# Kernel optimization log

Hardware: AMD Instinct MI355X
Metric: run time of the kernel (lower is better)

The kernel has to match this reference:

```python
import jax, jax.numpy as jnp
import numpy as np

LAMBDA_SOFTMAX = 20.0  # opt.lambda_softmax
EPS = 1e-8
NEG = -1e30


def l2norm(x, axis):
    # torch l2norm: x / (sqrt(sum x^2) + eps)
    n = jnp.sqrt(jnp.sum(x * x, axis=axis, keepdims=True)) + EPS
    return x / n


def cosine(x1, x2, axis):
    # torch compute_similarity: sum(x1*x2)/clamp(|x1||x2|, min=eps)
    w12 = jnp.sum(x1 * x2, axis=axis)
    w1 = jnp.sqrt(jnp.sum(x1 * x1, axis=axis))
    w2 = jnp.sqrt(jnp.sum(x2 * x2, axis=axis))
    return w12 / jnp.maximum(w1 * w2, EPS)


def _focal_renorm(a, sourceL):
    # focal_equal: fattn = 1[a*S - sum(a) > 0], then renormalize fattn*a
    funcF = a * sourceL - jnp.sum(a, axis=-1, keepdims=True)
    fattn = jnp.where(funcF > 0, 1.0, 0.0)
    ta = fattn * a
    s = jnp.sum(ta, axis=-1, keepdims=True)
    return ta / jnp.where(s > 0, s, 1.0)


def compute_weiTexts(img_q, img_v, txt_k_all, txt_v_all, text_length):
    N, R, d = img_q.shape          # n_img, n_region, d
    Lw = txt_k_all.shape[1]        # max words
    qn_img = l2norm(img_q, -1)     # [N,R,d]
    mask_all = (jnp.arange(Lw)[None, :] < text_length[:, None])  # [T,Lw] bool

    def per_text(txt_k, txt_v, mask, n_word):
        # mask out padded words (torch slices [:n_word])
        m = mask.astype(txt_k.dtype)[:, None]        # [Lw,1]
        tk = l2norm(txt_k * m, -1)                   # [Lw,d], padded rows -> 0
        tv = txt_v * m                                # [Lw,d]

        # ---- i2t: query=img, context=text (sourceL = n_word) ----
        attn = jnp.einsum('ld,nrd->nlr', tk, qn_img)  # bmm(key_norm, queryT) [N,Lw,R]
        attn = jax.nn.leaky_relu(attn, 0.1)
        attn = l2norm(attn, 2)                        # over R
        attn = jnp.transpose(attn, (0, 2, 1))         # [N,R,Lw]
        logits = jnp.where(mask[None, None, :], attn * LAMBDA_SOFTMAX, NEG)
        a = jax.nn.softmax(logits, axis=-1)           # [N,R,Lw]
        a = _focal_renorm(a, n_word)
        wei_text = jnp.einsum('nrl,ld->nrd', a, tv)   # [N,R,d]
        wei_text = l2norm(wei_text, 2)
        i2t = jnp.mean(cosine(img_v, wei_text, 2), axis=1)  # [N]

        # ---- t2i: query=text, context=img (sourceL = R) ----
        attn2 = jnp.einsum('nrd,ld->nrl', qn_img, tk)  # bmm(key_norm, queryT) [N,R,Lw]
        attn2 = jax.nn.leaky_relu(attn2, 0.1)
        attn2 = l2norm(attn2, 2)                       # over Lw (padded cols are 0)
        attn2 = jnp.transpose(attn2, (0, 2, 1))        # [N,Lw,R]
        a2 = jax.nn.softmax(attn2 * LAMBDA_SOFTMAX, axis=-1)
        a2 = _focal_renorm(a2, float(R))
        wei_img = jnp.einsum('nlr,nrd->nld', a2, img_v)  # [N,Lw,d]
        wei_img = l2norm(wei_img, 2)
        cos2 = cosine(tv[None, :, :], wei_img, 2)        # [N,Lw]; padded rows -> 0
        t2i = jnp.sum(cos2 * mask.astype(cos2.dtype)[None, :], axis=1) / n_word
        return i2t, t2i

    n_word_f = text_length.astype(img_q.dtype)
    i2t_T, t2i_T = jax.vmap(per_text)(txt_k_all, txt_v_all, mask_all, n_word_f)
    # loop concatenated along dim 1 -> [n_img, n_txt]
    return i2t_T.T, t2i_T.T


def setup_inputs() -> dict:
    key = jax.random.key(0)
    k1, k2, k3, k4, k5 = jax.random.split(key, 5)
    N, T, R, Lw, d = 128, 128, 48, 64, 1024
    return {
        'local_img_query': jax.random.normal(k1, (N, R, d), dtype=jnp.float32),
        'local_img_value': jax.random.normal(k2, (N, R, d), dtype=jnp.float32),
        'local_text_key': jax.random.normal(k3, (T, Lw, d), dtype=jnp.float32),
        'local_text_value': jax.random.normal(k4, (T, Lw, d), dtype=jnp.float32),
        'text_length': jax.random.randint(k5, (T,), 16, Lw + 1, dtype=jnp.int32),
    }


def reference(local_img_query, local_img_value, local_text_key, local_text_value, text_length):
    return compute_weiTexts(local_img_query, local_img_value,
                            local_text_key, local_text_value, text_length)
```

## Files before the change

kernel.cpp:

```cpp
#include <hip/hip_runtime.h>

#define NIMG 128
#define NTXT 128
#define RDIM 48
#define LWRD 64
#define DDIM 1024
#define LAMB 20.0f
#define FEPS 1e-8f

#define WS_INVQ 0
#define WS_VN   6144
#define WS_INVK 12288
#define WS_TVN  20480
#define WS_H    28672
#define WS_VG   552960
#define WS_MID_BYTES 3391488ull
#define WS_HU   847872
#define WS_VGU  1372160
#define SP_TK   3334144
#define SP_TV   20111360
#define SP_Q    36888576
#define SP_V    49471488
#define WS_BIG_BYTES 124108800ull

typedef unsigned int u32;
typedef __attribute__((ext_vector_type(8))) short short8;
typedef __attribute__((ext_vector_type(4))) float f32x4;
typedef __attribute__((ext_vector_type(4))) u32 uintx4;
typedef __attribute__((ext_vector_type(2))) u32 uintx2;

#define MFMA(a,b,c) __builtin_amdgcn_mfma_f32_16x16x32_bf16(a,b,c,0,0,0)

__device__ __forceinline__ u32 f2bf(float x){
    u32 u = __float_as_uint(x);
    return (u + 0x7fffu + ((u >> 16) & 1u)) >> 16;
}
__device__ __forceinline__ float bf2f(u32 h){ return __uint_as_float(h << 16); }
__device__ __forceinline__ u32 packsplit(float x){
    u32 h = f2bf(x);
    u32 l = f2bf(x - bf2f(h));
    return h | (l << 16);
}
__device__ __forceinline__ void unpk(uintx4 a, uintx4 b, short8& hi, short8& lo){
    uintx4 h, l;
    h.x = (a.x & 0xffffu) | (a.y << 16);
    h.y = (a.z & 0xffffu) | (a.w << 16);
    h.z = (b.x & 0xffffu) | (b.y << 16);
    h.w = (b.z & 0xffffu) | (b.w << 16);
    l.x = (a.x >> 16) | (a.y & 0xffff0000u);
    l.y = (a.z >> 16) | (a.w & 0xffff0000u);
    l.z = (b.x >> 16) | (b.y & 0xffff0000u);
    l.w = (b.z >> 16) | (b.w & 0xffff0000u);
    hi = __builtin_bit_cast(short8, h);
    lo = __builtin_bit_cast(short8, l);
}

#define PSTR  40
#define PTKH  0
#define PTVH  2560
#define PQH   5120
#define PVH   8960
#define LOGAP 12800
__device__ __forceinline__ void split_store(short* stg, int idx, float4 x, float sc){
    float a0 = x.x*sc, a1 = x.y*sc, a2 = x.z*sc, a3 = x.w*sc;
    u32 h0=f2bf(a0), h1=f2bf(a1), h2=f2bf(a2), h3=f2bf(a3);
    u32 l0=f2bf(a0-bf2f(h0)), l1=f2bf(a1-bf2f(h1)), l2=f2bf(a2-bf2f(h2)), l3=f2bf(a3-bf2f(h3));
    uintx2 hv; hv.x = h0 | (h1<<16); hv.y = h2 | (h3<<16);
    uintx2 lv; lv.x = l0 | (l1<<16); lv.y = l2 | (l3<<16);
    *(uintx2*)(stg + idx)         = hv;
    *(uintx2*)(stg + idx + LOGAP) = lv;
}
__device__ __forceinline__ short8 frag_ld(const short* stg, int plane, int rb, int m16, int quad){
    return *(const short8*)(stg + plane + (rb + m16) * PSTR + quad * 8);
}

__global__ __launch_bounds__(256, 2)
void prep_norms(const float* __restrict__ imq, const float* __restrict__ imv,
                const float* __restrict__ txk, const float* __restrict__ txv,
                float* __restrict__ ws) {
    int vid = blockIdx.x * 4 + (threadIdx.x >> 6);
    int lane = threadIdx.x & 63;
    const float* src;
    if (vid < 6144)       src = imq + (size_t)vid * 1024;
    else if (vid < 12288) src = imv + (size_t)(vid - 6144) * 1024;
    else if (vid < 20480) src = txk + (size_t)(vid - 12288) * 1024;
    else                  src = txv + (size_t)(vid - 20480) * 1024;
    const float4* s4 = (const float4*)src;
    float acc = 0.f;
#pragma unroll
    for (int j = 0; j < 4; ++j) {
        float4 v = s4[lane + 64 * j];
        acc += v.x * v.x + v.y * v.y + v.z * v.z + v.w * v.w;
    }
#pragma unroll
    for (int off = 32; off; off >>= 1) acc += __shfl_down(acc, off, 64);
    if (lane == 0) {
        float nrm = sqrtf(acc);
        if (vid < 6144)       ws[vid] = 1.f / (nrm + FEPS);
        else if (vid < 12288) ws[vid] = nrm;
        else if (vid < 20480) ws[vid] = 1.f / (nrm + FEPS);
        else                  ws[vid] = nrm;
    }
}

__global__ __launch_bounds__(256, 2)
void split_kernel(const float* __restrict__ imq, const float* __restrict__ imv,
                  const float* __restrict__ txk, const float* __restrict__ txv,
                  const int* __restrict__ tlen, const float* __restrict__ wsf,
                  short* __restrict__ wss) {
    const int ten = blockIdx.y;
    const int jid = blockIdx.x * 256 + threadIdx.x;
    const float* src; float sc; size_t dst; int psz;
    if (ten < 2) {
        int slab = jid >> 13, r = jid & 8191;
        int kc = r >> 8, row = (r >> 2) & 63, ks = r & 3;
        const float* base = (ten == 0) ? txk : txv;
        src = base + (size_t)slab * 65536 + row * 1024 + kc * 32 + ks * 8;
        int nw = tlen[slab];
        if (ten == 0) sc = (row < nw) ? wsf[WS_INVK + slab * 64 + row] : 0.f;
        else          sc = (row < nw) ? 1.f : 0.f;
        dst = (size_t)(ten == 0 ? SP_TK : SP_TV) + (size_t)slab * 131072
            + kc * 2048 + row * 32 + ks * 8;
        psz = 65536;
    } else {
        if (jid >= 786432) return;
        int slab = jid / 6144, r = jid - slab * 6144;
        int kc = r / 192; int rr = r - kc * 192;
        int row = rr >> 2, ks = rr & 3;
        const float* base = (ten == 2) ? imq : imv;
        src = base + (size_t)slab * 49152 + row * 1024 + kc * 32 + ks * 8;
        sc = (ten == 2) ? wsf[WS_INVQ + slab * 48 + row] : 1.f;
        dst = (size_t)(ten == 2 ? SP_Q : SP_V) + (size_t)slab * 98304
            + kc * 1536 + row * 32 + ks * 8;
        psz = 49152;
    }
    float4 x0 = *(const float4*)src;
    float4 x1 = *(const float4*)(src + 4);
    float v[8] = {x0.x, x0.y, x0.z, x0.w, x1.x, x1.y, x1.z, x1.w};
    short8 hv, lv;
#pragma unroll
    for (int i = 0; i < 8; ++i) {
        float a = v[i] * sc;
        u32 h = f2bf(a);
        hv[i] = (short)h;
        lv[i] = (short)f2bf(a - bf2f(h));
    }
    *(short8*)(wss + dst) = hv;
    *(short8*)(wss + dst + psz) = lv;
}

template <int TS>
__device__ __forceinline__ void gram_body(const float* __restrict__ src,
                                          float* __restrict__ dstf,
                                          u32* __restrict__ dstu,
                                          int mode, int nw, float* sT){
    const int NR = TS * 16;
    int ar = threadIdx.x >> 4, ac = threadIdx.x & 15;
    float acc[TS][TS];
#pragma unroll
    for (int i = 0; i < TS; ++i)
#pragma unroll
        for (int j = 0; j < TS; ++j) acc[i][j] = 0.f;
    for (int kc = 0; kc < 8; ++kc) {
        int k0 = kc * 128;
        for (int jid = threadIdx.x; jid < NR * 32; jid += 256) {
            int row = jid >> 5, c4 = jid & 31;
            float4 x = *(const float4*)(src + row * 1024 + k0 + c4 * 4);
            float sc = (row < nw) ? 1.f : 0.f;
            x.x *= sc; x.y *= sc; x.z *= sc; x.w *= sc;
            *(float4*)&sT[row * 132 + c4 * 4] = x;
        }
        __syncthreads();
#pragma unroll 4
        for (int k4 = 0; k4 < 32; ++k4) {
            float4 av[TS], bv[TS];
#pragma unroll
            for (int i = 0; i < TS; ++i) av[i] = *(const float4*)&sT[(TS*ar + i) * 132 + k4 * 4];
#pragma unroll
            for (int j = 0; j < TS; ++j) bv[j] = *(const float4*)&sT[(TS*ac + j) * 132 + k4 * 4];
#pragma unroll
            for (int i = 0; i < TS; ++i)
#pragma unroll
                for (int j = 0; j < TS; ++j)
                    acc[i][j] += av[i].x*bv[j].x + av[i].y*bv[j].y + av[i].z*bv[j].z + av[i].w*bv[j].w;
        }
        __syncthreads();
    }
#pragma unroll
    for (int i = 0; i < TS; ++i)
#pragma unroll
        for (int j = 0; j < TS; ++j) {
            int idx = (TS*ar + i) * NR + TS*ac + j;
            if (mode) dstu[idx] = packsplit(acc[i][j]);
            else      dstf[idx] = acc[i][j];
        }
}

__global__ __launch_bounds__(256, 2)
void gram_kernel(const float* __restrict__ txv, const float* __restrict__ imv,
                 const int* __restrict__ tlen, float* __restrict__ ws, int mode){
    __shared__ __align__(16) float sT[64 * 132];
    int b = blockIdx.x;
    u32* wsu = (u32*)ws;
    if (b < 128) {
        gram_body<4>(txv + (size_t)b * 65536, ws + WS_H + (size_t)b * 4096,
                     wsu + WS_HU + (size_t)b * 4096, mode, tlen[b], sT);
    } else {
        int n = b - 128;
        gram_body<3>(imv + (size_t)n * 49152, ws + WS_VG + (size_t)n * 2304,
                     wsu + WS_VGU + (size_t)n * 2304, mode, 48, sT);
    }
}

__global__ __launch_bounds__(256, 4)
void loss_mfma3(const int* __restrict__ tlen, const float* __restrict__ ws,
                float* __restrict__ out) {
    const int n    = blockIdx.x;
    const int t    = blockIdx.y;
    const int tid  = threadIdx.x;
    const int lane = tid & 63;
    const int w    = tid >> 6;
    const int quad = lane >> 4;
    const int m16  = lane & 15;

    __shared__ __align__(16) float Sm[10064];
    u32*   A1w = (u32*)Sm;
    u32*   A2w = ((u32*)Sm) + 3264;
    short* stg = (short*)Sm;
    float* P   = Sm + 6592;
    float* sNl = Sm + 9728;
    float* sNr = Sm + 9792;
    float* sD1 = Sm + 9840;
    float* sS1 = Sm + 9888;
    float* sD2 = Sm + 9936;
    float* sS2 = Sm + 10000;

    const int nw = tlen[t];
    const float nwf = (float)nw;
    const short* wss = (const short*)ws;
    const u32*   wsu = (const u32*)ws;

    const short* bsrc[3]; int bdst[3];
#pragma unroll
    for (int it = 0; it < 3; ++it) {
        int jid = tid + 256 * it;
        int p = jid / 192; int rr = jid - p * 192;
        int row = rr >> 2, ks = rr & 3;
        bsrc[it] = wss + (p < 2 ? SP_Q : SP_V) + (size_t)n * 98304
                 + (size_t)(p & 1) * 49152 + row * 32 + ks * 8;
        bdst[it] = p * 1920 + row * 40 + ks * 8;
    }

    const short* tkh = wss + SP_TK + (size_t)t * 131072;
    const short* tkl = tkh + 65536;
    const short* tvh = wss + SP_TV + (size_t)t * 131072;
    const short* tvl = tvh + 65536;
    const int ar = (16 * w + m16) * 32 + quad * 8;

    f32x4 accS[3], accG[3];
    f32x4 zf = {0.f, 0.f, 0.f, 0.f};
#pragma unroll
    for (int j = 0; j < 3; ++j) { accS[j] = zf; accG[j] = zf; }

    short8 bj[3];
#pragma unroll
    for (int it = 0; it < 3; ++it) bj[it] = *(const short8*)(bsrc[it]);
    short8 kh0, kl0, th0, tl0, kh1, kl1, th1, tl1;
    kh0 = *(const short8*)(tkh + ar); kl0 = *(const short8*)(tkl + ar);
    th0 = *(const short8*)(tvh + ar); tl0 = *(const short8*)(tvl + ar);

    for (int kc2 = 0; kc2 < 16; ++kc2) {
        const int kc = kc2 * 2;
        {
#pragma unroll
            for (int it = 0; it < 3; ++it) *(short8*)(stg + bdst[it]) = bj[it];
            __syncthreads();
            int bo = (kc + 1) * 1536, ao = (kc + 1) * 2048 + ar;
#pragma unroll
            for (int it = 0; it < 3; ++it) bj[it] = *(const short8*)(bsrc[it] + bo);
            kh1 = *(const short8*)(tkh + ao); kl1 = *(const short8*)(tkl + ao);
            th1 = *(const short8*)(tvh + ao); tl1 = *(const short8*)(tvl + ao);
#pragma unroll
            for (int j = 0; j < 3; ++j) {
                int o = (16 * j + m16) * 40 + quad * 8;
                short8 bqh = *(const short8*)(stg + o);
                short8 bql = *(const short8*)(stg + 1920 + o);
                short8 bvh = *(const short8*)(stg + 3840 + o);
                short8 bvl = *(const short8*)(stg + 5760 + o);
                accS[j] = MFMA(kh0, bqh, accS[j]);
                accS[j] = MFMA(kh0, bql, accS[j]);
                accS[j] = MFMA(kl0, bqh, accS[j]);
                accG[j] = MFMA(th0, bvh, accG[j]);
                accG[j] = MFMA(th0, bvl, accG[j]);
                accG[j] = MFMA(tl0, bvh, accG[j]);
            }
            __syncthreads();
        }
        {
#pragma unroll
            for (int it = 0; it < 3; ++it) *(short8*)(stg + bdst[it]) = bj[it];
            __syncthreads();
            if (kc2 < 15) {
                int bo = (kc + 2) * 1536, ao = (kc + 2) * 2048 + ar;
#pragma unroll
                for (int it = 0; it < 3; ++it) bj[it] = *(const short8*)(bsrc[it] + bo);
                kh0 = *(const short8*)(tkh + ao); kl0 = *(const short8*)(tkl + ao);
                th0 = *(const short8*)(tvh + ao); tl0 = *(const short8*)(tvl + ao);
            }
#pragma unroll
            for (int j = 0; j < 3; ++j) {
                int o = (16 * j + m16) * 40 + quad * 8;
                short8 bqh = *(const short8*)(stg + o);
                short8 bql = *(const short8*)(stg + 1920 + o);
                short8 bvh = *(const short8*)(stg + 3840 + o);
                short8 bvl = *(const short8*)(stg + 5760 + o);
                accS[j] = MFMA(kh1, bqh, accS[j]);
                accS[j] = MFMA(kh1, bql, accS[j]);
                accS[j] = MFMA(kl1, bqh, accS[j]);
                accG[j] = MFMA(th1, bvh, accG[j]);
                accG[j] = MFMA(th1, bvl, accG[j]);
                accG[j] = MFMA(tl1, bvh, accG[j]);
            }
            __syncthreads();
        }
    }

#pragma unroll
    for (int j = 0; j < 3; ++j)
#pragma unroll
        for (int v = 0; v < 4; ++v) {
            int l = 16 * w + quad * 4 + v;
            float x = accS[j][v];
            P[l * 49 + 16 * j + m16] = (x > 0.f) ? x : 0.1f * x;
        }
    __syncthreads();

    if (tid < 64) {
        float s = 0.f;
#pragma unroll 4
        for (int r = 0; r < 48; ++r) { float x = P[tid * 49 + r]; s += x * x; }
        sNl[tid] = sqrtf(s) + FEPS;
    } else if (tid < 112) {
        int r = tid - 64;
        float s = 0.f;
#pragma unroll 4
        for (int l = 0; l < 64; ++l) { float x = P[l * 49 + r]; s += x * x; }
        sNr[r] = sqrtf(s) + FEPS;
    } else if (tid < 208) {
        int k = tid - 112;
        if (k < 48) sD1[k] = 0.f; else sS1[k - 48] = 0.f;
    }
    __syncthreads();

    if (tid < 64) {
        int l = tid;
        u32* row = A2w + l * 52;
        if (l < nw) {
            float a[48]; float mx = -1e30f;
            const float* Pr = P + l * 49;
#pragma unroll
            for (int r = 0; r < 48; ++r) {
                float x = LAMB * Pr[r] / sNr[r];
                a[r] = x; mx = fmaxf(mx, x);
            }
            float se = 0.f;
#pragma unroll
            for (int r = 0; r < 48; ++r) { float e = __expf(a[r] - mx); a[r] = e; se += e; }
            float suma = 0.f;
#pragma unroll
            for (int r = 0; r < 48; ++r) { float x = a[r] / se; a[r] = x; suma += x; }
            float s2 = 0.f;
#pragma unroll
            for (int r = 0; r < 48; ++r) if (a[r] * 48.f - suma > 0.f) s2 += a[r];
            float ri = (s2 > 0.f) ? 1.f / s2 : 1.f;
#pragma unroll
            for (int r = 0; r < 48; ++r) {
                float x = (a[r] * 48.f - suma > 0.f) ? a[r] * ri : 0.f;
                row[r] = packsplit(x);
            }
        } else {
#pragma unroll
            for (int r = 0; r < 48; ++r) row[r] = 0u;
        }
    } else if (tid < 112) {
        int r = tid - 64;
        float a[64]; float mx = -1e30f;
#pragma unroll
        for (int l = 0; l < 64; ++l) {
            float x = (l < nw) ? (LAMB * P[l * 49 + r] / sNl[l]) : -1e30f;
            a[l] = x; mx = fmaxf(mx, x);
        }
        float se = 0.f;
#pragma unroll
        for (int l = 0; l < 64; ++l) { float e = __expf(a[l] - mx); a[l] = e; se += e; }
        float suma = 0.f;
#pragma unroll
        for (int l = 0; l < 64; ++l) { float x = a[l] / se; a[l] = x; suma += x; }
        float s2 = 0.f;
#pragma unroll
        for (int l = 0; l < 64; ++l) if (a[l] * nwf - suma > 0.f) s2 += a[l];
        float ri = (s2 > 0.f) ? 1.f / s2 : 1.f;
        u32* row = A1w + r * 68;
#pragma unroll
        for (int l = 0; l < 64; ++l) {
            float x = (a[l] * nwf - suma > 0.f) ? a[l] * ri : 0.f;
            row[l] = packsplit(x);
        }
    }
    __syncthreads();

    f32x4 accY[3];
#pragma unroll
    for (int j = 0; j < 3; ++j) accY[j] = zf;
    const u32* Hg = wsu + WS_HU + (size_t)t * 4096 + (16 * w + m16) * 64;
#pragma unroll
    for (int ks = 0; ks < 2; ++ks) {
        int kb = ks * 32 + quad * 8;
        short8 Ah, Al;
        {
            uintx4 wa = *(const uintx4*)&Hg[kb];
            uintx4 wb = *(const uintx4*)&Hg[kb + 4];
            unpk(wa, wb, Ah, Al);
        }
#pragma unroll
        for (int j = 0; j < 3; ++j) {
            int base = (16 * j + m16) * 68 + kb;
            uintx4 wa = *(const uintx4*)&A1w[base];
            uintx4 wb = *(const uintx4*)&A1w[base + 4];
            short8 Bh, Bl;
            unpk(wa, wb, Bh, Bl);
            accY[j] = MFMA(Ah, Bh, accY[j]);
            accY[j] = MFMA(Ah, Bl, accY[j]);
            accY[j] = MFMA(Al, Bh, accY[j]);
        }
    }
    {
        float td[3] = {0.f, 0.f, 0.f}, ts[3] = {0.f, 0.f, 0.f};
#pragma unroll
        for (int v = 0; v < 4; ++v) {
            int l = 16 * w + quad * 4 + v;
#pragma unroll
            for (int j = 0; j < 3; ++j) {
                u32 wv = A1w[(16 * j + m16) * 68 + l];
                float av = bf2f(wv & 0xffffu) + bf2f(wv >> 16);
                td[j] += av * accG[j][v];
                ts[j] += av * accY[j][v];
            }
        }
#pragma unroll
        for (int j = 0; j < 3; ++j) {
            float d = td[j]; d += __shfl_xor(d, 16, 64); d += __shfl_xor(d, 32, 64);
            float s = ts[j]; s += __shfl_xor(s, 16, 64); s += __shfl_xor(s, 32, 64);
            if (quad == 0) {
                atomicAdd(&sD1[16 * j + m16], d);
                atomicAdd(&sS1[16 * j + m16], s);
            }
        }
    }

    f32x4 accY2[3];
#pragma unroll
    for (int i = 0; i < 3; ++i) accY2[i] = zf;
    const u32* Vgg = wsu + WS_VGU + (size_t)n * 2304;
#pragma unroll
    for (int ks = 0; ks < 2; ++ks) {
        const bool dead = (ks == 1) && (quad >= 2);
        const int kb = (ks == 0) ? quad * 8 : 32 + (quad & 1) * 8;
        short8 Bh2, Bl2;
        {
            uintx4 wa = {0,0,0,0}, wb = {0,0,0,0};
            if (!dead) {
                int base = (16 * w + m16) * 52 + kb;
                wa = *(const uintx4*)&A2w[base];
                wb = *(const uintx4*)&A2w[base + 4];
            }
            unpk(wa, wb, Bh2, Bl2);
        }
#pragma unroll
        for (int i = 0; i < 3; ++i) {
            uintx4 wa = {0,0,0,0}, wb = {0,0,0,0};
            if (!dead) {
                wa = *(const uintx4*)&Vgg[(16 * i + m16) * 48 + kb];
                wb = *(const uintx4*)&Vgg[(16 * i + m16) * 48 + kb + 4];
            }
            short8 Ah2, Al2;
            unpk(wa, wb, Ah2, Al2);
            accY2[i] = MFMA(Ah2, Bh2, accY2[i]);
            accY2[i] = MFMA(Ah2, Bl2, accY2[i]);
            accY2[i] = MFMA(Al2, Bh2, accY2[i]);
        }
    }
    {
        float u = 0.f;
#pragma unroll
        for (int i = 0; i < 3; ++i)
#pragma unroll
            for (int v = 0; v < 4; ++v) {
                int r = 16 * i + quad * 4 + v;
                u32 wv = A2w[(16 * w + m16) * 52 + r];
                float av = bf2f(wv & 0xffffu) + bf2f(wv >> 16);
                u += av * accY2[i][v];
            }
        u += __shfl_xor(u, 16, 64); u += __shfl_xor(u, 32, 64);
        if (quad == 0) sS2[16 * w + m16] = u;
        float ud[4] = {0.f, 0.f, 0.f, 0.f};
#pragma unroll
        for (int v = 0; v < 4; ++v) {
            int l = 16 * w + quad * 4 + v;
#pragma unroll
            for (int j = 0; j < 3; ++j) {
                u32 wv = A2w[l * 52 + 16 * j + m16];
                float av = bf2f(wv & 0xffffu) + bf2f(wv >> 16);
                ud[v] += av * accG[j][v];
            }
        }
#pragma unroll
        for (int v = 0; v < 4; ++v) {
            float d = ud[v];
            d += __shfl_xor(d, 1, 64); d += __shfl_xor(d, 2, 64);
            d += __shfl_xor(d, 4, 64); d += __shfl_xor(d, 8, 64);
            if (m16 == 0) sD2[16 * w + quad * 4 + v] = d;
        }
    }
    __syncthreads();

    if (tid < 48) {
        int r = tid;
        float wn = sqrtf(sS1[r]);
        float dh = sD1[r] / (wn + FEPS);
        float nh = wn / (wn + FEPS);
        float vn = ws[WS_VN + n * 48 + r];
        sD1[r] = dh / fmaxf(vn * nh, FEPS);
    } else if (tid >= 64 && tid < 128) {
        int l = tid - 64;
        if (l < nw) {
            float wn = sqrtf(sS2[l]);
            float dh = sD2[l] / (wn + FEPS);
            float nh = wn / (wn + FEPS);
            float tn = ws[WS_TVN + t * 64 + l];
            sD2[l] = dh / fmaxf(tn * nh, FEPS);
        }
    }
    __syncthreads();
    if (tid == 0) {
        float s = 0.f;
        for (int r = 0; r < 48; ++r) s += sD1[r];
        out[(size_t)n * NTXT + t] = s / 48.f;
    } else if (tid == 64) {
        float s = 0.f;
        for (int l = 0; l < nw; ++l) s += sD2[l];
        out[(size_t)(NIMG * NTXT) + (size_t)n * NTXT + t] = s / nwf;
    }
}

__global__ __launch_bounds__(256, 2)
void loss_mfma(const float* __restrict__ imq, const float* __restrict__ imv,
               const float* __restrict__ txk, const float* __restrict__ txv,
               const int* __restrict__ tlen, const float* __restrict__ ws,
               float* __restrict__ out) {
    const int npair = blockIdx.x;
    const int t     = blockIdx.y;
    const int n0    = npair * 2;
    const int tid   = threadIdx.x;
    const int lane  = tid & 63;
    const int w     = tid >> 6;
    const int nl    = w >> 1;
    const int hh    = w & 1;
    const int quad  = lane >> 4;
    const int m16   = lane & 15;

    __shared__ __align__(16) float Sm[19904];
    short* stage = (short*)Sm;
    u32*   A1w   = (u32*)Sm;
    u32*   A2w   = ((u32*)Sm) + 6528;
    float* P     = Sm + 12800;
    u32*   HVw   = (u32*)(Sm + 12800);
    float* sInvK = Sm + 19072;
    float* sInvQ = sInvK + 64;
    float* sNl   = sInvQ + 96;
    float* sNr   = sNl + 128;
    float* sD1   = sNr + 96;
    float* sS1   = sD1 + 96;
    float* sD2   = sS1 + 96;
    float* sS2   = sD2 + 128;

    const int nw = tlen[t];
    const float nwf = (float)nw;
    if (tid < 64) sInvK[tid] = ws[WS_INVK + t * 64 + tid];
    else if (tid < 160) {
        int i = tid - 64; int nn = i >= 48; int r = i - 48 * nn;
        sInvQ[i] = ws[WS_INVQ + (n0 + nn) * 48 + r];
    }
    __syncthreads();

    const float* tkb = txk + (size_t)t * 65536;
    const float* tvb = txv + (size_t)t * 65536;
    const float* qb0 = imq + (size_t)n0 * 49152;
    const float* vb0 = imv + (size_t)n0 * 49152;

    const float* sp[10]; int di[10]; float scl[10];
#pragma unroll
    for (int it = 0; it < 10; ++it) {
        int jid = tid + 256 * it;
        const float* s; int plane; int row, c4; float sc;
        if (it < 2) {
            row = jid >> 3; c4 = jid & 7;
            s = tkb + row * 1024 + c4 * 4;
            sc = (row < nw) ? sInvK[row] : 0.f;
            plane = PTKH;
        } else if (it < 4) {
            int j2 = jid - 512; row = j2 >> 3; c4 = j2 & 7;
            s = tvb + row * 1024 + c4 * 4;
            sc = (row < nw) ? 1.f : 0.f;
            plane = PTVH;
        } else if (it < 7) {
            int j2 = jid - 1024; row = j2 >> 3; c4 = j2 & 7;
            s = qb0 + row * 1024 + c4 * 4;
            sc = sInvQ[row];
            plane = PQH;
        } else {
            int j2 = jid - 1792; row = j2 >> 3; c4 = j2 & 7;
            s = vb0 + row * 1024 + c4 * 4;
            sc = 1.f;
            plane = PVH;
        }
        sp[it] = s; di[it] = plane + row * PSTR + c4 * 4; scl[it] = sc;
    }

    f32x4 accS[2][3], accG[2][3];
    f32x4 zf = {0.f, 0.f, 0.f, 0.f};
#pragma unroll
    for (int i = 0; i < 2; ++i)
#pragma unroll
        for (int j = 0; j < 3; ++j) { accS[i][j] = zf; accG[i][j] = zf; }

    float4 pf[10];
#pragma unroll
    for (int it = 0; it < 10; ++it) pf[it] = *(const float4*)(sp[it]);

    for (int kc = 0; kc < 32; ++kc) {
#pragma unroll
        for (int it = 0; it < 10; ++it) split_store(stage, di[it], pf[it], scl[it]);
        __syncthreads();
        if (kc < 31) {
            const int ko = (kc + 1) * 32;
#pragma unroll
            for (int it = 0; it < 10; ++it) pf[it] = *(const float4*)(sp[it] + ko);
        }
        short8 akh[2], akl[2], ath[2], atl[2];
#pragma unroll
        for (int i = 0; i < 2; ++i) {
            int rb = 32 * hh + 16 * i;
            akh[i] = frag_ld(stage, PTKH,         rb, m16, quad);
            akl[i] = frag_ld(stage, PTKH + LOGAP, rb, m16, quad);
            ath[i] = frag_ld(stage, PTVH,         rb, m16, quad);
            atl[i] = frag_ld(stage, PTVH + LOGAP, rb, m16, quad);
        }
        short8 bqh[3], bql[3], bvh[3], bvl[3];
#pragma unroll
        for (int j = 0; j < 3; ++j) {
            int rb = nl * 48 + 16 * j;
            bqh[j] = frag_ld(stage, PQH,         rb, m16, quad);
            bql[j] = frag_ld(stage, PQH + LOGAP, rb, m16, quad);
            bvh[j] = frag_ld(stage, PVH,         rb, m16, quad);
            bvl[j] = frag_ld(stage, PVH + LOGAP, rb, m16, quad);
        }
#pragma unroll
        for (int i = 0; i < 2; ++i)
#pragma unroll
            for (int j = 0; j < 3; ++j) {
                accS[i][j] = MFMA(akh[i], bqh[j], accS[i][j]);
                accS[i][j] = MFMA(akh[i], bql[j], accS[i][j]);
                accS[i][j] = MFMA(akl[i], bqh[j], accS[i][j]);
                accG[i][j] = MFMA(ath[i], bvh[j], accG[i][j]);
                accG[i][j] = MFMA(ath[i], bvl[j], accG[i][j]);
                accG[i][j] = MFMA(atl[i], bvh[j], accG[i][j]);
            }
        __syncthreads();
    }

#pragma unroll
    for (int i = 0; i < 2; ++i)
#pragma unroll
        for (int j = 0; j < 3; ++j)
#pragma unroll
            for (int v = 0; v < 4; ++v) {
                int l = 32 * hh + 16 * i + quad * 4 + v;
                int r = 16 * j + m16;
                float x = accS[i][j][v];
                P[nl * 3136 + l * 49 + r] = (x > 0.f) ? x : 0.1f * x;
            }
    __syncthreads();

    if (tid < 128) {
        int n = tid >> 6, l = tid & 63;
        float s = 0.f;
#pragma unroll 4
        for (int r = 0; r < 48; ++r) { float x = P[n*3136 + l*49 + r]; s += x * x; }
        sNl[n * 64 + l] = sqrtf(s) + FEPS;
    } else if (tid < 224) {
        int i = tid - 128; int n = i >= 48; int r = i - 48 * n;
        float s = 0.f;
#pragma unroll 4
        for (int l = 0; l < 64; ++l) { float x = P[n*3136 + l*49 + r]; s += x * x; }
        sNr[n * 48 + r] = sqrtf(s) + FEPS;
    } else {
        for (int k = tid - 224; k < 448; k += 32) sD1[k] = 0.f;
    }
    __syncthreads();

    if (tid < 128) {
        int n = tid >> 6, l = tid & 63;
        u32* row = A2w + n * 3072 + l * 48;
        if (l < nw) {
            float a[48]; float mx = -1e30f;
            const float* Pr = P + n * 3136 + l * 49;
#pragma unroll
            for (int r = 0; r < 48; ++r) {
                float x = LAMB * Pr[r] / sNr[n * 48 + r];
                a[r] = x; mx = fmaxf(mx, x);
            }
            float se = 0.f;
#pragma unroll
            for (int r = 0; r < 48; ++r) { float e = __expf(a[r] - mx); a[r] = e; se += e; }
            float suma = 0.f;
#pragma unroll
            for (int r = 0; r < 48; ++r) { float x = a[r] / se; a[r] = x; suma += x; }
            float s2 = 0.f;
#pragma unroll
            for (int r = 0; r < 48; ++r) if (a[r] * 48.f - suma > 0.f) s2 += a[r];
            float ri = (s2 > 0.f) ? 1.f / s2 : 1.f;
#pragma unroll
            for (int r = 0; r < 48; ++r) {
                float x = (a[r] * 48.f - suma > 0.f) ? a[r] * ri : 0.f;
                row[r] = packsplit(x);
            }
        } else {
#pragma unroll
            for (int r = 0; r < 48; ++r) row[r] = 0u;
        }
    } else if (tid < 224) {
        int i = tid - 128; int n = i >= 48; int r = i - 48 * n;
        float a[64]; float mx = -1e30f;
#pragma unroll
        for (int l = 0; l < 64; ++l) {
            float x = (l < nw) ? (LAMB * P[n*3136 + l*49 + r] / sNl[n * 64 + l]) : -1e30f;
            a[l] = x; mx = fmaxf(mx, x);
        }
        float se = 0.f;
#pragma unroll
        for (int l = 0; l < 64; ++l) { float e = __expf(a[l] - mx); a[l] = e; se += e; }
        float suma = 0.f;
#pragma unroll
        for (int l = 0; l < 64; ++l) { float x = a[l] / se; a[l] = x; suma += x; }
        float s2 = 0.f;
#pragma unroll
        for (int l = 0; l < 64; ++l) if (a[l] * nwf - suma > 0.f) s2 += a[l];
        float ri = (s2 > 0.f) ? 1.f / s2 : 1.f;
        u32* row = A1w + n * 3264 + r * 68;
#pragma unroll
        for (int l = 0; l < 64; ++l) {
            float x = (a[l] * nwf - suma > 0.f) ? a[l] * ri : 0.f;
            row[l] = packsplit(x);
        }
    }
    __syncthreads();

    {
        const float* Hg = ws + WS_H + (size_t)t * 4096;
        for (int jid = tid; jid < 1024; jid += 256) {
            int row = jid >> 4, c4 = jid & 15;
            float4 x = *(const float4*)(Hg + row * 64 + c4 * 4);
            uintx4 p; p.x = packsplit(x.x); p.y = packsplit(x.y);
            p.z = packsplit(x.z); p.w = packsplit(x.w);
            *(uintx4*)&HVw[row * 68 + c4 * 4] = p;
        }
    }
    __syncthreads();

    f32x4 accY[2][3];
#pragma unroll
    for (int i = 0; i < 2; ++i)
#pragma unroll
        for (int j = 0; j < 3; ++j) accY[i][j] = zf;
#pragma unroll
    for (int ks = 0; ks < 2; ++ks) {
        int kb = ks * 32 + quad * 8;
        short8 Ah[2], Al[2];
#pragma unroll
        for (int i = 0; i < 2; ++i) {
            int row = 32 * hh + 16 * i + m16;
            uintx4 wa = *(const uintx4*)&HVw[row * 68 + kb];
            uintx4 wb = *(const uintx4*)&HVw[row * 68 + kb + 4];
            unpk(wa, wb, Ah[i], Al[i]);
        }
        short8 Bh[3], Bl[3];
#pragma unroll
        for (int j = 0; j < 3; ++j) {
            int base = nl * 3264 + (16 * j + m16) * 68 + kb;
            uintx4 wa = *(const uintx4*)&A1w[base];
            uintx4 wb = *(const uintx4*)&A1w[base + 4];
            unpk(wa, wb, Bh[j], Bl[j]);
        }
#pragma unroll
        for (int i = 0; i < 2; ++i)
#pragma unroll
            for (int j = 0; j < 3; ++j) {
                accY[i][j] = MFMA(Ah[i], Bh[j], accY[i][j]);
                accY[i][j] = MFMA(Ah[i], Bl[j], accY[i][j]);
                accY[i][j] = MFMA(Al[i], Bh[j], accY[i][j]);
            }
    }
    {
        float td[3] = {0.f, 0.f, 0.f}, ts[3] = {0.f, 0.f, 0.f};
#pragma unroll
        for (int i = 0; i < 2; ++i)
#pragma unroll
            for (int v = 0; v < 4; ++v) {
                int l = 32 * hh + 16 * i + quad * 4 + v;
#pragma unroll
                for (int j = 0; j < 3; ++j) {
                    u32 wv = A1w[nl * 3264 + (16 * j + m16) * 68 + l];
                    float av = bf2f(wv & 0xffffu) + bf2f(wv >> 16);
                    td[j] += av * accG[i][j][v];
                    ts[j] += av * accY[i][j][v];
                }
            }
#pragma unroll
        for (int j = 0; j < 3; ++j) {
            float d = td[j]; d += __shfl_xor(d, 16, 64); d += __shfl_xor(d, 32, 64);
            float s = ts[j]; s += __shfl_xor(s, 16, 64); s += __shfl_xor(s, 32, 64);
            if (quad == 0) {
                atomicAdd(&sD1[nl * 48 + 16 * j + m16], d);
                atomicAdd(&sS1[nl * 48 + 16 * j + m16], s);
            }
        }
    }
    __syncthreads();

    {
        const float* Vgg = ws + WS_VG + (size_t)n0 * 2304;
        for (int jid = tid; jid < 1152; jid += 256) {
            int nn = jid >= 576; int j2 = jid - 576 * nn;
            int row = j2 / 12, c4 = j2 % 12;
            float4 x = *(const float4*)(Vgg + nn * 2304 + row * 48 + c4 * 4);
            uintx4 p; p.x = packsplit(x.x); p.y = packsplit(x.y);
            p.z = packsplit(x.z); p.w = packsplit(x.w);
            *(uintx4*)&HVw[nn * 2496 + row * 52 + c4 * 4] = p;
        }
    }
    __syncthreads();

    f32x4 accY2[3][2];
#pragma unroll
    for (int i = 0; i < 3; ++i)
#pragma unroll
        for (int j = 0; j < 2; ++j) accY2[i][j] = zf;
    const u32* VgW = HVw + nl * 2496;
#pragma unroll
    for (int ks = 0; ks < 2; ++ks) {
        const bool dead = (ks == 1) && (quad >= 2);
        const int kb = (ks == 0) ? quad * 8 : 32 + (quad & 1) * 8;
        short8 Ah2[3], Al2[3];
#pragma unroll
        for (int i = 0; i < 3; ++i) {
            uintx4 wa = {0,0,0,0}, wb = {0,0,0,0};
            if (!dead) {
                int row = 16 * i + m16;
                wa = *(const uintx4*)&VgW[row * 52 + kb];
                wb = *(const uintx4*)&VgW[row * 52 + kb + 4];
            }
            unpk(wa, wb, Ah2[i], Al2[i]);
        }
        short8 Bh2[2], Bl2[2];
#pragma unroll
        for (int j = 0; j < 2; ++j) {
            uintx4 wa = {0,0,0,0}, wb = {0,0,0,0};
            if (!dead) {
                int l = 32 * hh + 16 * j + m16;
                wa = *(const uintx4*)&A2w[nl * 3072 + l * 48 + kb];
                wb = *(const uintx4*)&A2w[nl * 3072 + l * 48 + kb + 4];
            }
            unpk(wa, wb, Bh2[j], Bl2[j]);
        }
#pragma unroll
        for (int i = 0; i < 3; ++i)
#pragma unroll
            for (int j = 0; j < 2; ++j) {
                accY2[i][j] = MFMA(Ah2[i], Bh2[j], accY2[i][j]);
                accY2[i][j] = MFMA(Ah2[i], Bl2[j], accY2[i][j]);
                accY2[i][j] = MFMA(Al2[i], Bh2[j], accY2[i][j]);
            }
    }
    {
        float u[2] = {0.f, 0.f};
#pragma unroll
        for (int i = 0; i < 3; ++i)
#pragma unroll
            for (int v = 0; v < 4; ++v) {
                int r = 16 * i + quad * 4 + v;
#pragma unroll
                for (int j = 0; j < 2; ++j) {
                    int l = 32 * hh + 16 * j + m16;
                    u32 wv = A2w[nl * 3072 + l * 48 + r];
                    float av = bf2f(wv & 0xffffu) + bf2f(wv >> 16);
                    u[j] += av * accY2[i][j][v];
                }
            }
#pragma unroll
        for (int j = 0; j < 2; ++j) {
            float s = u[j]; s += __shfl_xor(s, 16, 64); s += __shfl_xor(s, 32, 64);
            if (quad == 0) sS2[nl * 64 + 32 * hh + 16 * j + m16] = s;
        }
        float ud[2][4];
#pragma unroll
        for (int i = 0; i < 2; ++i)
#pragma unroll
            for (int v = 0; v < 4; ++v) ud[i][v] = 0.f;
#pragma unroll
        for (int i = 0; i < 2; ++i)
#pragma unroll
            for (int v = 0; v < 4; ++v) {
                int l = 32 * hh + 16 * i + quad * 4 + v;
#pragma unroll
                for (int j = 0; j < 3; ++j) {
                    u32 wv = A2w[nl * 3072 + l * 48 + (16 * j + m16)];
                    float av = bf2f(wv & 0xffffu) + bf2f(wv >> 16);
                    ud[i][v] += av * accG[i][j][v];
                }
            }
#pragma unroll
        for (int i = 0; i < 2; ++i)
#pragma unroll
            for (int v = 0; v < 4; ++v) {
                float d = ud[i][v];
                d += __shfl_xor(d, 1, 64); d += __shfl_xor(d, 2, 64);
                d += __shfl_xor(d, 4, 64); d += __shfl_xor(d, 8, 64);
                if (m16 == 0) sD2[nl * 64 + 32 * hh + 16 * i + quad * 4 + v] = d;
            }
    }
    __syncthreads();

    if (tid < 96) {
        int n = tid >= 48; int r = tid - 48 * n;
        float wn = sqrtf(sS1[n * 48 + r]);
        float dh = sD1[n * 48 + r] / (wn + FEPS);
        float nh = wn / (wn + FEPS);
        float vn = ws[WS_VN + (n0 + n) * 48 + r];
        sD1[n * 48 + r] = dh / fmaxf(vn * nh, FEPS);
    } else if (tid >= 128) {
        int i = tid - 128; int n = i >> 6, l = i & 63;
        if (l < nw) {
            float wn = sqrtf(sS2[n * 64 + l]);
            float dh = sD2[n * 64 + l] / (wn + FEPS);
            float nh = wn / (wn + FEPS);
            float tn = ws[WS_TVN + t * 64 + l];
            sD2[n * 64 + l] = dh / fmaxf(tn * nh, FEPS);
        }
    }
    __syncthreads();
    if (tid < 2) {
        float s = 0.f;
        for (int r = 0; r < 48; ++r) s += sD1[tid * 48 + r];
        out[(size_t)(n0 + tid) * NTXT + t] = s / 48.f;
    } else if (tid == 64 || tid == 65) {
        int n = tid - 64;
        float s = 0.f;
        for (int l = 0; l < nw; ++l) s += sD2[n * 64 + l];
        out[(size_t)(NIMG * NTXT) + (size_t)(n0 + n) * NTXT + t] = s / nwf;
    }
}

extern "C" void kernel_launch(void* const* d_in, const int* in_sizes, int n_in,
                              void* d_out, int out_size, void* d_ws, size_t ws_size,
                              hipStream_t stream) {
    (void)in_sizes; (void)n_in; (void)out_size;
    const float* imq = (const float*)d_in[0];
    const float* imv = (const float*)d_in[1];
    const float* txk = (const float*)d_in[2];
    const float* txv = (const float*)d_in[3];
    const int*   tln = (const int*)d_in[4];
    float* out = (float*)d_out;
    float* ws  = (float*)d_ws;

    prep_norms<<<7168, 256, 0, stream>>>(imq, imv, txk, txv, ws);
    if (ws_size >= WS_BIG_BYTES) {
        split_kernel<<<dim3(4096, 4), 256, 0, stream>>>(imq, imv, txk, txv, tln,
                                                        ws, (short*)d_ws);
        gram_kernel<<<256, 256, 0, stream>>>(txv, imv, tln, ws, 1);
        dim3 grid(NIMG, NTXT);
        loss_mfma3<<<grid, 256, 0, stream>>>(tln, ws, out);
    } else {
        gram_kernel<<<256, 256, 0, stream>>>(txv, imv, tln, ws, 0);
        dim3 grid(64, 128);
        loss_mfma<<<grid, 256, 0, stream>>>(imq, imv, txk, txv, tln, ws, out);
    }
}
```

Measured before the change: 1.063 ms.

## Stream image tiles into double-buffered LDS via global_load_lds with swizzled layout

The image query/value bf16 split tiles in the loss kernel are now copied straight from global memory into LDS with the gfx950 global_load_lds DMA, instead of passing through registers and then LDS stores. LDS staging becomes two buffers that alternate between chunks, which removes one of the two barriers per chunk. The padded row stride of 40 shorts is replaced by an unpadded stride of 32. To keep LDS reads free of bank conflicts, the split kernel now writes the image planes with an XOR swizzle and the reader applies the matching XOR. This depends on the compiler placing correct vmcnt waits before the barriers, since the DMA writes LDS asynchronously.

```diff
diff --git a/kernel.cpp b/kernel.cpp
--- a/kernel.cpp
+++ b/kernel.cpp
@@ -53,6 +53,12 @@
     l.w = (b.z >> 16) | (b.w & 0xffff0000u);
     hi = __builtin_bit_cast(short8, h);
     lo = __builtin_bit_cast(short8, l);
+}
+
+__device__ __forceinline__ void dma16(const short* g, short* l){
+    __builtin_amdgcn_global_load_lds(
+        (const __attribute__((address_space(1))) void*)g,
+        (__attribute__((address_space(3))) void*)l, 16, 0, 0);
 }
 
 #define PSTR  40
@@ -130,8 +136,9 @@
         const float* base = (ten == 2) ? imq : imv;
         src = base + (size_t)slab * 49152 + row * 1024 + kc * 32 + ks * 8;
         sc = (ten == 2) ? wsf[WS_INVQ + slab * 48 + row] : 1.f;
+        int ksw = ks ^ ((row >> 1) & 3);
         dst = (size_t)(ten == 2 ? SP_Q : SP_V) + (size_t)slab * 98304
-            + kc * 1536 + row * 32 + ks * 8;
+            + kc * 1536 + row * 32 + ksw * 8;
         psz = 49152;
     }
     float4 x0 = *(const float4*)src;
@@ -213,7 +220,7 @@
 }
 
 __global__ __launch_bounds__(256, 4)
-void loss_mfma3(const int* __restrict__ tlen, const float* __restrict__ ws,
+void loss_mfma4(const int* __restrict__ tlen, const float* __restrict__ ws,
                 float* __restrict__ out) {
     const int n    = blockIdx.x;
     const int t    = blockIdx.y;
@@ -240,31 +247,28 @@
     const short* wss = (const short*)ws;
     const u32*   wsu = (const u32*)ws;
 
-    const short* bsrc[3]; int bdst[3];
-#pragma unroll
-    for (int it = 0; it < 3; ++it) {
-        int jid = tid + 256 * it;
-        int p = jid / 192; int rr = jid - p * 192;
-        int row = rr >> 2, ks = rr & 3;
-        bsrc[it] = wss + (p < 2 ? SP_Q : SP_V) + (size_t)n * 98304
-                 + (size_t)(p & 1) * 49152 + row * 32 + ks * 8;
-        bdst[it] = p * 1920 + row * 40 + ks * 8;
-    }
+    const short* qh = wss + SP_Q + (size_t)n * 98304;
+    const short* vh = wss + SP_V + (size_t)n * 98304;
+    const short* mp = (w == 0) ? qh : (w == 1) ? (qh + 49152)
+                   : (w == 2) ? vh : (vh + 49152);
 
     const short* tkh = wss + SP_TK + (size_t)t * 131072;
     const short* tkl = tkh + 65536;
     const short* tvh = wss + SP_TV + (size_t)t * 131072;
     const short* tvl = tvh + 65536;
     const int ar = (16 * w + m16) * 32 + quad * 8;
+    const int swq = (quad ^ ((m16 >> 1) & 3)) * 8;
 
     f32x4 accS[3], accG[3];
     f32x4 zf = {0.f, 0.f, 0.f, 0.f};
 #pragma unroll
     for (int j = 0; j < 3; ++j) { accS[j] = zf; accG[j] = zf; }
 
-    short8 bj[3];
-#pragma unroll
-    for (int it = 0; it < 3; ++it) bj[it] = *(const short8*)(bsrc[it]);
+    {
+        const short* gs = mp + lane * 8;
+        short* ld = stg + w * 1536;
+        dma16(gs, ld); dma16(gs + 512, ld + 512); dma16(gs + 1024, ld + 1024);
+    }
     short8 kh0, kl0, th0, tl0, kh1, kl1, th1, tl1;
     kh0 = *(const short8*)(tkh + ar); kl0 = *(const short8*)(tkl + ar);
     th0 = *(const short8*)(tvh + ar); tl0 = *(const short8*)(tvl + ar);
@@ -272,21 +276,22 @@
     for (int kc2 = 0; kc2 < 16; ++kc2) {
         const int kc = kc2 * 2;
         {
-#pragma unroll
-            for (int it = 0; it < 3; ++it) *(short8*)(stg + bdst[it]) = bj[it];
             __syncthreads();
-            int bo = (kc + 1) * 1536, ao = (kc + 1) * 2048 + ar;
-#pragma unroll
-            for (int it = 0; it < 3; ++it) bj[it] = *(const short8*)(bsrc[it] + bo);
+            {
+                const short* gs = mp + (kc + 1) * 1536 + lane * 8;
+                short* ld = stg + 6144 + w * 1536;
+                dma16(gs, ld); dma16(gs + 512, ld + 512); dma16(gs + 1024, ld + 1024);
+            }
+            int ao = (kc + 1) * 2048 + ar;
             kh1 = *(const short8*)(tkh + ao); kl1 = *(const short8*)(tkl + ao);
             th1 = *(const short8*)(tvh + ao); tl1 = *(const short8*)(tvl + ao);
 #pragma unroll
             for (int j = 0; j < 3; ++j) {
-                int o = (16 * j + m16) * 40 + quad * 8;
-                short8 bqh = *(const short8*)(stg + o);
-                short8 bql = *(const short8*)(stg + 1920 + o);
-                short8 bvh = *(const short8*)(stg + 3840 + o);
-                short8 bvl = *(const short8*)(stg + 5760 + o);
+                int rb = (16 * j + m16) * 32 + swq;
+                short8 bqh = *(const short8*)(stg + rb);
+                short8 bql = *(const short8*)(stg + rb + 1536);
+                short8 bvh = *(const short8*)(stg + rb + 3072);
+                short8 bvl = *(const short8*)(stg + rb + 4608);
                 accS[j] = MFMA(kh0, bqh, accS[j]);
                 accS[j] = MFMA(kh0, bql, accS[j]);
                 accS[j] = MFMA(kl0, bqh, accS[j]);
@@ -294,26 +299,24 @@
                 accG[j] = MFMA(th0, bvl, accG[j]);
                 accG[j] = MFMA(tl0, bvh, accG[j]);
             }
-            __syncthreads();
         }
         {
-#pragma unroll
-            for (int it = 0; it < 3; ++it) *(short8*)(stg + bdst[it]) = bj[it];
             __syncthreads();
             if (kc2 < 15) {
-                int bo = (kc + 2) * 1536, ao = (kc + 2) * 2048 + ar;
-#pragma unroll
-                for (int it = 0; it < 3; ++it) bj[it] = *(const short8*)(bsrc[it] + bo);
+                const short* gs = mp + (kc + 2) * 1536 + lane * 8;
+                short* ld = stg + w * 1536;
+                dma16(gs, ld); dma16(gs + 512, ld + 512); dma16(gs + 1024, ld + 1024);
+                int ao = (kc + 2) * 2048 + ar;
                 kh0 = *(const short8*)(tkh + ao); kl0 = *(const short8*)(tkl + ao);
                 th0 = *(const short8*)(tvh + ao); tl0 = *(const short8*)(tvl + ao);
             }
 #pragma unroll
             for (int j = 0; j < 3; ++j) {
-                int o = (16 * j + m16) * 40 + quad * 8;
-                short8 bqh = *(const short8*)(stg + o);
-                short8 bql = *(const short8*)(stg + 1920 + o);
-                short8 bvh = *(const short8*)(stg + 3840 + o);
-                short8 bvl = *(const short8*)(stg + 5760 + o);
+                int rb = 6144 + (16 * j + m16) * 32 + swq;
+                short8 bqh = *(const short8*)(stg + rb);
+                short8 bql = *(const short8*)(stg + rb + 1536);
+                short8 bvh = *(const short8*)(stg + rb + 3072);
+                short8 bvl = *(const short8*)(stg + rb + 4608);
                 accS[j] = MFMA(kh1, bqh, accS[j]);
                 accS[j] = MFMA(kh1, bql, accS[j]);
                 accS[j] = MFMA(kl1, bqh, accS[j]);
@@ -321,9 +324,9 @@
                 accG[j] = MFMA(th1, bvl, accG[j]);
                 accG[j] = MFMA(tl1, bvh, accG[j]);
             }
-            __syncthreads();
-        }
-    }
+        }
+    }
+    __syncthreads();
 
 #pragma unroll
     for (int j = 0; j < 3; ++j)
@@ -989,7 +992,7 @@
                                                         ws, (short*)d_ws);
         gram_kernel<<<256, 256, 0, stream>>>(txv, imv, tln, ws, 1);
         dim3 grid(NIMG, NTXT);
-        loss_mfma3<<<grid, 256, 0, stream>>>(tln, ws, out);
+        loss_mfma4<<<grid, 256, 0, stream>>>(tln, ws, out);
     } else {
         gram_kernel<<<256, 256, 0, stream>>>(txv, imv, tln, ws, 0);
         dim3 grid(64, 128);
```

Measured after the change: 1.116 ms. 1.05x slower.
